# Optimization experiments

Hardware: AMD Instinct MI355X
Metric: run time of the kernel (lower is better)

Reference implementation:

```python
import jax, jax.numpy as jnp
import numpy as np

N_NODES = 100000
N_EDGES = 600000
D = 128          # encoder_output_dim
H = 64           # mlp_edge_model_dim


def setup_inputs() -> dict:
    key = jax.random.key(0)
    k1, k2, k3, k4, k5, k6 = jax.random.split(key, 6)
    node_emb = jax.random.normal(k1, (N_NODES, D), dtype=jnp.float32)
    edge_index = jax.random.randint(k2, (2, N_EDGES), 0, N_NODES, dtype=jnp.int64)
    # MLP params (Linear(2D -> H), Linear(H -> 1)); scale ~ PyTorch default init
    s1 = 1.0 / np.sqrt(2 * D)
    s2 = 1.0 / np.sqrt(H)
    W1 = jax.random.uniform(k3, (2 * D, H), dtype=jnp.float32, minval=-s1, maxval=s1)
    b1 = jax.random.uniform(k4, (H,), dtype=jnp.float32, minval=-s1, maxval=s1)
    W2 = jax.random.uniform(k5, (H, 1), dtype=jnp.float32, minval=-s2, maxval=s2)
    b2 = jax.random.uniform(k6, (1,), dtype=jnp.float32, minval=-s2, maxval=s2)
    return {"node_emb": node_emb, "edge_index": edge_index,
            "W1": W1, "b1": b1, "W2": W2, "b2": b2}


def reference(node_emb, edge_index, W1, b1, W2, b2):
    src, dst = edge_index[0], edge_index[1]
    emb_src = node_emb[src]                      # [E, D] gather
    emb_dst = node_emb[dst]                      # [E, D] gather
    edge_emb = jnp.concatenate([emb_src, emb_dst], axis=1)  # [E, 2D]
    h = jax.nn.relu(edge_emb @ W1 + b1)          # [E, H]
    edge_logits = h @ W2 + b2                    # [E, 1]
    return edge_logits
```

## Files before the change

### kernel.cpp

```cpp
#include <hip/hip_runtime.h>
#include <hip/hip_fp16.h>

#define N_NODES 100000
#define N_EDGES 600000
#define DIM 128
#define HID 64
#define NTILES 6250

typedef __attribute__((ext_vector_type(8))) _Float16 half8;
typedef __attribute__((ext_vector_type(4))) _Float16 half4v;
typedef __attribute__((ext_vector_type(4))) float floatx4;

#define VMCNT(n) asm volatile("s_waitcnt vmcnt(" #n ")" ::: "memory")

__device__ __forceinline__ void gload_lds16(const void* g, void* l) {
    __builtin_amdgcn_global_load_lds(
        (const __attribute__((address_space(1))) void*)g,
        (__attribute__((address_space(3))) void*)l, 16, 0, 0);
}

__global__ __launch_bounds__(256) void prep_W(
    const float* __restrict__ W1, __half* __restrict__ W1T)
{
    const int o = (int)(blockIdx.x * blockDim.x + threadIdx.x) * 2;
    if (o >= 128 * 128) return;
    const int c = o >> 7, k = o & 127;
    float w0, w1;
    if (c < HID) { w0 = W1[k * HID + c];               w1 = W1[(k + 1) * HID + c]; }
    else         { w0 = W1[(DIM + k) * HID + c - HID]; w1 = W1[(DIM + k + 1) * HID + c - HID]; }
    W1T[o]     = __float2half(w0);
    W1T[o + 1] = __float2half(w1);
}

__global__ __launch_bounds__(256, 2) void precompute_P(
    const float* __restrict__ node_emb,
    const __half* __restrict__ W1T,
    const float* __restrict__ b1,
    __half* __restrict__ P)
{
    __shared__ char lds[4][2][8192];

    const int tid  = threadIdx.x;
    const int w    = tid >> 6;
    const int lane = tid & 63;
    const int lr   = lane & 15;
    const int q    = lane >> 4;

    half8 wf[8][4];
#pragma unroll
    for (int nt = 0; nt < 8; nt++)
#pragma unroll
        for (int ks = 0; ks < 4; ks++)
            wf[nt][ks] = *(const half8*)(W1T + (size_t)(nt * 16 + lr) * 128 + ks * 32 + q * 8);

    float bias_[4][4];
#pragma unroll
    for (int nt = 0; nt < 4; nt++) {
        const float4 b4 = *(const float4*)(b1 + nt * 16 + q * 4);
        bias_[nt][0] = b4.x; bias_[nt][1] = b4.y;
        bias_[nt][2] = b4.z; bias_[nt][3] = b4.w;
    }

    const int b     = (int)blockIdx.x;
    const int base  = b * 12 + (b < 106 ? b : 106);
    const int quota = 12 + (b < 106 ? 1 : 0);

    const char* nb = (const char*)node_emb;
    char* const bufs[2] = { &lds[w][0][0], &lds[w][1][0] };

    const int rhalf = lane >> 5;
    const int in16  = (lane & 31) << 4;

#define STAGE(T, BUF)                                                        \
    {                                                                        \
        _Pragma("unroll")                                                    \
        for (int r = 0; r < 8; r++) {                                        \
            const int row_in = 2 * r + rhalf;                                \
            const size_t src = (size_t)((T) * 16 + row_in) * 512             \
                             + (size_t)(in16 ^ ((row_in & 7) << 4));         \
            gload_lds16(nb + src, (BUF) + r * 1024);                         \
        }                                                                    \
    }

    int i  = w;
    int tA = (i     < quota) ? base + i     : -1;
    int tB = (i + 4 < quota) ? base + i + 4 : -1;
    int nexti = i + 8;

    if (tA >= 0) STAGE(tA, bufs[0]);
    if (tB >= 0) STAGE(tB, bufs[1]);

    int cur = 0;
    bool first = true;
    while (tA >= 0) {
        if (first) { if (tB >= 0) VMCNT(8);  else VMCNT(0); }
        else       { if (tB >= 0) VMCNT(12); else VMCNT(4); }

        floatx4 acc[8];
#pragma unroll
        for (int nt = 0; nt < 8; nt++) acc[nt] = (floatx4){0.f, 0.f, 0.f, 0.f};

        const char* Ab = bufs[cur];
        const int sw = (lr & 7) << 4;
#pragma unroll
        for (int ks = 0; ks < 4; ks++) {
            const int cb = ks * 128 + q * 32;
            const float4 x0 = *(const float4*)(Ab + lr * 512 + ((cb)      ^ sw));
            const float4 x1 = *(const float4*)(Ab + lr * 512 + ((cb + 16) ^ sw));
            half8 af;
            af[0] = (_Float16)x0.x; af[1] = (_Float16)x0.y;
            af[2] = (_Float16)x0.z; af[3] = (_Float16)x0.w;
            af[4] = (_Float16)x1.x; af[5] = (_Float16)x1.y;
            af[6] = (_Float16)x1.z; af[7] = (_Float16)x1.w;
#pragma unroll
            for (int nt = 0; nt < 8; nt++)
                acc[nt] = __builtin_amdgcn_mfma_f32_16x16x32_f16(wf[nt][ks], af, acc[nt], 0, 0, 0);
        }

        asm volatile("s_waitcnt lgkmcnt(0)" ::: "memory");
        __builtin_amdgcn_sched_barrier(0);

        const int tC = (nexti < quota) ? base + nexti : -1;
        if (tC >= 0) STAGE(tC, bufs[cur]);

        {
            char* prow = (char*)P + (size_t)(tA * 16 + lr) * 256;
#pragma unroll
            for (int m = 0; m < 4; m++) {
                half8 hh;
#pragma unroll
                for (int ii = 0; ii < 4; ii++) {
                    float va = acc[2 * m][ii];
                    float vb = acc[2 * m + 1][ii];
                    if (m < 2) { va += bias_[2 * m][ii]; vb += bias_[2 * m + 1][ii]; }
                    hh[ii]     = (_Float16)va;
                    hh[ii + 4] = (_Float16)vb;
                }
                *(half8*)(prow + m * 64 + q * 16) = hh;
            }
        }

        tA = tB; tB = tC; nexti += 4; cur ^= 1; first = false;
    }
#undef STAGE
}

__device__ inline bool detect_int64(const int* e32) {
    int orv = 0;
#pragma unroll
    for (int k = 0; k < 8; k++) orv |= e32[2 * k + 1];
    return orv == 0;
}

__global__ __launch_bounds__(256) void edge_mlp(
    const __half* __restrict__ P,
    const void* __restrict__ eidx_raw,
    const float* __restrict__ W2,
    const float* __restrict__ b2,
    float* __restrict__ out)
{
    const int* e32 = (const int*)eidx_raw;
    const long long* e64 = (const long long*)eidx_raw;
    const bool is64 = detect_int64(e32);

    const int tid  = threadIdx.x;
    const int lane = tid & 63;
    const int j    = lane & 15;
    const int grp  = lane >> 4;
    const int hbase = ((j >> 3) << 5) + ((j & 1) << 4) + (((j >> 1) & 3) << 2);
    const float4 w2 = *(const float4*)(W2 + hbase);
    const float b2v = b2[0];

    const int gwid   = (int)((blockIdx.x * blockDim.x + tid) >> 6);
    const int nwaves = (int)((gridDim.x * blockDim.x) >> 6);

    const half4v zero = {(_Float16)0, (_Float16)0, (_Float16)0, (_Float16)0};

    for (int base = gwid * 16; base < N_EDGES; base += nwaves * 16) {
        int s[4], d[4];
#pragma unroll
        for (int u = 0; u < 4; u++) {
            const int e = base + 4 * u + grp;
            if (is64) { s[u] = (int)e64[e]; d[u] = (int)e64[N_EDGES + e]; }
            else      { s[u] = e32[e];      d[u] = e32[N_EDGES + e]; }
        }
        half4v av[4], bv[4];
#pragma unroll
        for (int u = 0; u < 4; u++) {
            av[u] = *(const half4v*)(P + (size_t)s[u] * 128 + 4 * j);
            bv[u] = *(const half4v*)(P + (size_t)d[u] * 128 + 64 + 4 * j);
        }
#pragma unroll
        for (int u = 0; u < 4; u++) {
            const half4v t = av[u] + bv[u];
            const half4v r = __builtin_elementwise_max(t, zero);
            float acc = (float)r[0] * w2.x + (float)r[1] * w2.y
                      + (float)r[2] * w2.z + (float)r[3] * w2.w;
#pragma unroll
            for (int off = 8; off >= 1; off >>= 1)
                acc += __shfl_xor(acc, off, 64);
            if (j == 0) out[base + 4 * u + grp] = acc + b2v;
        }
    }
}

__global__ __launch_bounds__(256) void edge_mlp_direct(
    const float* __restrict__ node_emb,
    const void* __restrict__ eidx_raw,
    const float* __restrict__ W1,
    const float* __restrict__ b1,
    const float* __restrict__ W2,
    const float* __restrict__ b2,
    float* __restrict__ out)
{
    const int* e32 = (const int*)eidx_raw;
    const long long* e64 = (const long long*)eidx_raw;
    const bool is64 = detect_int64(e32);

    const int lane = threadIdx.x & 63;
    const float w2  = W2[lane];
    const float b2v = b2[0];
    const int gwid   = (int)((blockIdx.x * blockDim.x + threadIdx.x) >> 6);
    const int nwaves = (int)((gridDim.x * blockDim.x) >> 6);

    for (int e = gwid; e < N_EDGES; e += nwaves) {
        int s, d;
        if (is64) { s = (int)e64[e]; d = (int)e64[N_EDGES + e]; }
        else      { s = e32[e];      d = e32[N_EDGES + e]; }
        const float* es = node_emb + (size_t)s * DIM;
        const float* ed = node_emb + (size_t)d * DIM;
        float acc = b1[lane];
        for (int k = 0; k < DIM; k++) {
            acc += es[k] * W1[k * HID + lane];
            acc += ed[k] * W1[(DIM + k) * HID + lane];
        }
        float t = fmaxf(acc, 0.f) * w2;
#pragma unroll
        for (int off = 32; off >= 1; off >>= 1)
            t += __shfl_xor(t, off, 64);
        if (lane == 0) out[e] = t + b2v;
    }
}

extern "C" void kernel_launch(void* const* d_in, const int* in_sizes, int n_in,
                              void* d_out, int out_size, void* d_ws, size_t ws_size,
                              hipStream_t stream) {
    const float* node_emb = (const float*)d_in[0];
    const void*  eidx     = d_in[1];
    const float* W1       = (const float*)d_in[2];
    const float* b1       = (const float*)d_in[3];
    const float* W2       = (const float*)d_in[4];
    const float* b2       = (const float*)d_in[5];
    float* out = (float*)d_out;

    const size_t wt_off = 32u * 1024 * 1024;
    const size_t need   = wt_off + 128 * 128 * sizeof(__half);

    if (ws_size >= need) {
        __half* P   = (__half*)d_ws;
        __half* W1T = (__half*)((char*)d_ws + wt_off);
        prep_W<<<32, 256, 0, stream>>>(W1, W1T);
        precompute_P<<<512, 256, 0, stream>>>(node_emb, W1T, b1, P);
        edge_mlp<<<2048, 256, 0, stream>>>(P, eidx, W2, b2, out);
    } else {
        edge_mlp_direct<<<4096, 256, 0, stream>>>(node_emb, eidx, W1, b1, W2, b2, out);
    }
}
```

Measured before the change: 51.57 us.

## Split precompute output columns across wave pairs and narrow edge gather to half2

precompute_P now assigns two waves per 16-row tile, with each wave computing half of the 128 output columns. This halves the per-wave weight-fragment registers, allows 4 blocks per CU and doubles the grid, and staging uses block-wide barriers with a shared double buffer. edge_mlp now processes 2 edges per wave-half using 32 lanes with half2 loads and a 32-lane reduction. The aim is higher occupancy and better gather efficiency, at the cost of extra barriers and shuffles.

After: 54.40 us. +5.5%, slower.

```diff
diff --git a/kernel.cpp b/kernel.cpp
--- a/kernel.cpp
+++ b/kernel.cpp
@@ -5,7 +5,7 @@
 #define N_EDGES 600000
 #define DIM 128
 #define HID 64
-#define NTILES 6250
+#define NPAIRS 3125
 
 typedef __attribute__((ext_vector_type(8))) _Float16 half8;
 typedef __attribute__((ext_vector_type(4))) _Float16 half4v;
@@ -32,75 +32,82 @@
     W1T[o + 1] = __float2half(w1);
 }
 
-__global__ __launch_bounds__(256, 2) void precompute_P(
+__global__ __launch_bounds__(256, 4) void precompute_P(
     const float* __restrict__ node_emb,
     const __half* __restrict__ W1T,
     const float* __restrict__ b1,
     __half* __restrict__ P)
 {
-    __shared__ char lds[4][2][8192];
+    __shared__ char lds[2][2][8192];
 
     const int tid  = threadIdx.x;
     const int w    = tid >> 6;
     const int lane = tid & 63;
     const int lr   = lane & 15;
     const int q    = lane >> 4;
-
-    half8 wf[8][4];
-#pragma unroll
-    for (int nt = 0; nt < 8; nt++)
+    const int s    = w >> 1;
+    const int ch   = w & 1;
+
+    half8 wf[4][4];
+#pragma unroll
+    for (int nt = 0; nt < 4; nt++)
 #pragma unroll
         for (int ks = 0; ks < 4; ks++)
-            wf[nt][ks] = *(const half8*)(W1T + (size_t)(nt * 16 + lr) * 128 + ks * 32 + q * 8);
+            wf[nt][ks] = *(const half8*)(W1T + (size_t)(ch * 64 + nt * 16 + lr) * 128 + ks * 32 + q * 8);
 
     float bias_[4][4];
 #pragma unroll
     for (int nt = 0; nt < 4; nt++) {
-        const float4 b4 = *(const float4*)(b1 + nt * 16 + q * 4);
-        bias_[nt][0] = b4.x; bias_[nt][1] = b4.y;
-        bias_[nt][2] = b4.z; bias_[nt][3] = b4.w;
+        if (ch == 0) {
+            const float4 b4 = *(const float4*)(b1 + nt * 16 + q * 4);
+            bias_[nt][0] = b4.x; bias_[nt][1] = b4.y;
+            bias_[nt][2] = b4.z; bias_[nt][3] = b4.w;
+        } else {
+            bias_[nt][0] = bias_[nt][1] = bias_[nt][2] = bias_[nt][3] = 0.f;
+        }
     }
 
     const int b     = (int)blockIdx.x;
-    const int base  = b * 12 + (b < 106 ? b : 106);
-    const int quota = 12 + (b < 106 ? 1 : 0);
-
-    const char* nb = (const char*)node_emb;
-    char* const bufs[2] = { &lds[w][0][0], &lds[w][1][0] };
-
+    const int base  = b * 3 + (b < 53 ? b : 53);
+    const int quota = 3 + (b < 53 ? 1 : 0);
+
+    const char* nb  = (const char*)node_emb;
+    const int h8    = w & 1;
     const int rhalf = lane >> 5;
     const int in16  = (lane & 31) << 4;
 
-#define STAGE(T, BUF)                                                        \
+#define STAGE(PI, B)                                                         \
     {                                                                        \
         _Pragma("unroll")                                                    \
-        for (int r = 0; r < 8; r++) {                                        \
-            const int row_in = 2 * r + rhalf;                                \
-            const size_t src = (size_t)((T) * 16 + row_in) * 512             \
+        for (int r = 0; r < 4; r++) {                                        \
+            const int row_in = h8 * 8 + 2 * r + rhalf;                       \
+            const size_t src = (size_t)((2 * (PI) + s) * 16 + row_in) * 512  \
                              + (size_t)(in16 ^ ((row_in & 7) << 4));         \
-            gload_lds16(nb + src, (BUF) + r * 1024);                         \
+            gload_lds16(nb + src,                                            \
+                        &lds[B][s][0] + h8 * 4096 + r * 1024);               \
         }                                                                    \
     }
 
-    int i  = w;
-    int tA = (i     < quota) ? base + i     : -1;
-    int tB = (i + 4 < quota) ? base + i + 4 : -1;
-    int nexti = i + 8;
-
-    if (tA >= 0) STAGE(tA, bufs[0]);
-    if (tB >= 0) STAGE(tB, bufs[1]);
+    int pi = base;
+    STAGE(pi, 0);
 
     int cur = 0;
     bool first = true;
-    while (tA >= 0) {
-        if (first) { if (tB >= 0) VMCNT(8);  else VMCNT(0); }
-        else       { if (tB >= 0) VMCNT(12); else VMCNT(4); }
-
-        floatx4 acc[8];
-#pragma unroll
-        for (int nt = 0; nt < 8; nt++) acc[nt] = (floatx4){0.f, 0.f, 0.f, 0.f};
-
-        const char* Ab = bufs[cur];
+    for (; pi < base + quota; pi++, cur ^= 1, first = false) {
+        const bool has_next = (pi + 1 < base + quota);
+        if (has_next) {
+            STAGE(pi + 1, cur ^ 1);
+            if (first) { VMCNT(4); } else { VMCNT(6); }
+        } else {
+            VMCNT(0);
+        }
+        __builtin_amdgcn_s_barrier();
+
+        floatx4 acc[4];
+#pragma unroll
+        for (int nt = 0; nt < 4; nt++) acc[nt] = (floatx4){0.f, 0.f, 0.f, 0.f};
+
+        const char* Ab = &lds[cur][s][0];
         const int sw = (lr & 7) << 4;
 #pragma unroll
         for (int ks = 0; ks < 4; ks++) {
@@ -113,34 +120,30 @@
             af[4] = (_Float16)x1.x; af[5] = (_Float16)x1.y;
             af[6] = (_Float16)x1.z; af[7] = (_Float16)x1.w;
 #pragma unroll
-            for (int nt = 0; nt < 8; nt++)
+            for (int nt = 0; nt < 4; nt++)
                 acc[nt] = __builtin_amdgcn_mfma_f32_16x16x32_f16(wf[nt][ks], af, acc[nt], 0, 0, 0);
         }
 
         asm volatile("s_waitcnt lgkmcnt(0)" ::: "memory");
         __builtin_amdgcn_sched_barrier(0);
 
-        const int tC = (nexti < quota) ? base + nexti : -1;
-        if (tC >= 0) STAGE(tC, bufs[cur]);
-
         {
-            char* prow = (char*)P + (size_t)(tA * 16 + lr) * 256;
-#pragma unroll
-            for (int m = 0; m < 4; m++) {
+            char* prow = (char*)P + (size_t)((2 * pi + s) * 16 + lr) * 256;
+#pragma unroll
+            for (int mm = 0; mm < 2; mm++) {
+                const int m = 2 * ch + mm;
                 half8 hh;
 #pragma unroll
                 for (int ii = 0; ii < 4; ii++) {
-                    float va = acc[2 * m][ii];
-                    float vb = acc[2 * m + 1][ii];
-                    if (m < 2) { va += bias_[2 * m][ii]; vb += bias_[2 * m + 1][ii]; }
+                    const float va = acc[2 * mm][ii]     + bias_[2 * mm][ii];
+                    const float vb = acc[2 * mm + 1][ii] + bias_[2 * mm + 1][ii];
                     hh[ii]     = (_Float16)va;
                     hh[ii + 4] = (_Float16)vb;
                 }
                 *(half8*)(prow + m * 64 + q * 16) = hh;
             }
         }
-
-        tA = tB; tB = tC; nexti += 4; cur ^= 1; first = false;
+        __builtin_amdgcn_s_barrier();
     }
 #undef STAGE
 }
@@ -165,41 +168,44 @@
 
     const int tid  = threadIdx.x;
     const int lane = tid & 63;
-    const int j    = lane & 15;
-    const int grp  = lane >> 4;
-    const int hbase = ((j >> 3) << 5) + ((j & 1) << 4) + (((j >> 1) & 3) << 2);
-    const float4 w2 = *(const float4*)(W2 + hbase);
+    const int sub  = lane >> 5;
+    const int j2   = lane & 31;
+    const int hb = ((j2 >> 4) * 2 + ((j2 >> 1) & 1)) * 16
+                 + (((j2 >> 2) & 3) << 2) + ((j2 & 1) << 1);
+    const float w2x = W2[hb];
+    const float w2y = W2[hb + 1];
     const float b2v = b2[0];
+    const __half2* P2 = (const __half2*)P;
 
     const int gwid   = (int)((blockIdx.x * blockDim.x + tid) >> 6);
     const int nwaves = (int)((gridDim.x * blockDim.x) >> 6);
 
-    const half4v zero = {(_Float16)0, (_Float16)0, (_Float16)0, (_Float16)0};
-
-    for (int base = gwid * 16; base < N_EDGES; base += nwaves * 16) {
+    for (int base = gwid * 8; base < N_EDGES; base += nwaves * 8) {
         int s[4], d[4];
 #pragma unroll
         for (int u = 0; u < 4; u++) {
-            const int e = base + 4 * u + grp;
+            const int e = base + 2 * u + sub;
             if (is64) { s[u] = (int)e64[e]; d[u] = (int)e64[N_EDGES + e]; }
             else      { s[u] = e32[e];      d[u] = e32[N_EDGES + e]; }
         }
-        half4v av[4], bv[4];
+        __half2 av[4], bv[4];
 #pragma unroll
         for (int u = 0; u < 4; u++) {
-            av[u] = *(const half4v*)(P + (size_t)s[u] * 128 + 4 * j);
-            bv[u] = *(const half4v*)(P + (size_t)d[u] * 128 + 64 + 4 * j);
+            av[u] = P2[(size_t)s[u] * 64 + j2];
+            bv[u] = P2[(size_t)d[u] * 64 + 32 + j2];
         }
 #pragma unroll
         for (int u = 0; u < 4; u++) {
-            const half4v t = av[u] + bv[u];
-            const half4v r = __builtin_elementwise_max(t, zero);
-            float acc = (float)r[0] * w2.x + (float)r[1] * w2.y
-                      + (float)r[2] * w2.z + (float)r[3] * w2.w;
-#pragma unroll
-            for (int off = 8; off >= 1; off >>= 1)
-                acc += __shfl_xor(acc, off, 64);
-            if (j == 0) out[base + 4 * u + grp] = acc + b2v;
+            const float2 a = __half22float2(av[u]);
+            const float2 b = __half22float2(bv[u]);
+            float t = fmaxf(a.x + b.x, 0.f) * w2x
+                    + fmaxf(a.y + b.y, 0.f) * w2y;
+#pragma unroll
+            for (int off = 16; off >= 1; off >>= 1)
+                t += __shfl_xor(t, off, 64);
+            const float o1 = __shfl(t, 32, 64);
+            if (lane == 0)
+                *(float2*)(out + base + 2 * u) = make_float2(t + b2v, o1 + b2v);
         }
     }
 }
@@ -260,7 +266,7 @@
         __half* P   = (__half*)d_ws;
         __half* W1T = (__half*)((char*)d_ws + wt_off);
         prep_W<<<32, 256, 0, stream>>>(W1, W1T);
-        precompute_P<<<512, 256, 0, stream>>>(node_emb, W1T, b1, P);
+        precompute_P<<<1024, 256, 0, stream>>>(node_emb, W1T, b1, P);
         edge_mlp<<<2048, 256, 0, stream>>>(P, eidx, W2, b2, out);
     } else {
         edge_mlp_direct<<<4096, 256, 0, stream>>>(node_emb, eidx, W1, b1, W2, b2, out);
```
